# Kernel tuning notes

Measured on AMD Instinct MI355X. Metric: run time of the kernel, lower is better.

Reference implementation:

```python
import jax, jax.numpy as jnp
import numpy as np
import math

B, S, E, H, FF = 2, 2048, 1024, 16, 4096
HD = E // H
EPS = 1e-6


def layer_norm(x, gamma, beta):
    mu = jnp.mean(x, axis=-1, keepdims=True)
    var = jnp.mean(jnp.square(x - mu), axis=-1, keepdims=True)
    return (x - mu) * jax.lax.rsqrt(var + EPS) * gamma + beta


def setup_inputs() -> dict:
    key = jax.random.key(0)
    ks = jax.random.split(key, 8)
    x_embeds = jax.random.normal(ks[0], (B, S, E), dtype=jnp.float32)
    # causal mask: True means masked (j > i), broadcastable over batch/heads
    mask = jnp.triu(jnp.ones((S, S), dtype=bool), k=1)[None, None]
    sc = 1.0 / math.sqrt(E)
    w_kqv = jax.random.normal(ks[1], (3 * E, E), dtype=jnp.float32) * sc
    w_o = jax.random.normal(ks[2], (E, E), dtype=jnp.float32) * sc
    w_up = jax.random.normal(ks[3], (FF, E), dtype=jnp.float32) * sc
    b_up = jnp.zeros((FF,), dtype=jnp.float32)
    w_down = jax.random.normal(ks[4], (E, FF), dtype=jnp.float32) / math.sqrt(FF)
    b_down = jnp.zeros((E,), dtype=jnp.float32)
    g1 = jnp.ones((E,), dtype=jnp.float32)
    b1 = jnp.zeros((E,), dtype=jnp.float32)
    g2 = jnp.ones((E,), dtype=jnp.float32)
    b2 = jnp.zeros((E,), dtype=jnp.float32)
    return {"x_embeds": x_embeds, "mask": mask, "w_kqv": w_kqv, "w_o": w_o,
            "w_up": w_up, "b_up": b_up, "w_down": w_down, "b_down": b_down,
            "g1": g1, "b1": b1, "g2": g2, "b2": b2}


def reference(x_embeds, mask, w_kqv, w_o, w_up, b_up, w_down, b_down, g1, b1, g2, b2):
    b, s = x_embeds.shape[0], x_embeds.shape[1]
    # --- attention ---
    kqv = x_embeds @ w_kqv.T                      # [B,S,3E]
    kqv = kqv.reshape(b, s, 3, H, HD).transpose(0, 3, 2, 1, 4)  # [B,H,3,S,HD]
    xk, xq, xv = kqv[:, :, 0], kqv[:, :, 1], kqv[:, :, 2]
    attn = jnp.einsum('bhqd,bhkd->bhqk', xq, xk) / math.sqrt(HD)
    attn = jnp.where(mask, -jnp.inf, attn)
    attn = jax.nn.softmax(attn, axis=-1)
    out = jnp.einsum('bhqk,bhkd->bhqd', attn, xv)  # [B,H,S,HD]
    out = out.transpose(0, 2, 1, 3).reshape(b, s, E)
    out = out @ w_o.T
    x = layer_norm(out + x_embeds, g1, b1)
    # --- ffnn ---
    h = jax.nn.relu(x @ w_up.T + b_up)
    h = h @ w_down.T + b_down
    return layer_norm(h + x, g2, b2)
```

## Files before the change

kernel.cpp:

```cpp
#include <hip/hip_runtime.h>
#include <stdint.h>

#define B_ 2
#define S_ 2048
#define E_ 1024
#define H_ 16
#define HD_ 64
#define FF_ 4096
#define M_ 4096
#define LOG2E_ 1.44269504f

typedef short bf16x8 __attribute__((ext_vector_type(8)));
typedef float f32x4  __attribute__((ext_vector_type(4)));
typedef short shortx4 __attribute__((ext_vector_type(4)));

#define MFMA16(a,b,c) __builtin_amdgcn_mfma_f32_16x16x32_bf16(a,b,c,0,0,0)

__device__ __forceinline__ short f2bf(float f) {
  uint32_t u = __builtin_bit_cast(uint32_t, f);
  u += 0x7fffu + ((u >> 16) & 1u);
  return (short)(u >> 16);
}
__device__ __forceinline__ float bf2f(short b) {
  uint32_t u = ((uint32_t)(uint16_t)b) << 16;
  return __builtin_bit_cast(float, u);
}
__device__ __forceinline__ float exp2_hw(float x) {
  float r;
  asm("v_exp_f32 %0, %1" : "=v"(r) : "v"(x));
  return r;
}

template<int CTRL>
__device__ __forceinline__ float dpp_ror(float x) {
  return __builtin_bit_cast(float,
    __builtin_amdgcn_update_dpp(0, __builtin_bit_cast(int, x), CTRL, 0xF, 0xF, true));
}
__device__ __forceinline__ float dpp_max16(float v) {
  v = fmaxf(v, dpp_ror<0x128>(v));
  v = fmaxf(v, dpp_ror<0x124>(v));
  v = fmaxf(v, dpp_ror<0x122>(v));
  v = fmaxf(v, dpp_ror<0x121>(v));
  return v;
}
__device__ __forceinline__ float dpp_sum16(float v) {
  v += dpp_ror<0x128>(v);
  v += dpp_ror<0x124>(v);
  v += dpp_ror<0x122>(v);
  v += dpp_ror<0x121>(v);
  return v;
}

#define GLDS16(g, l) __builtin_amdgcn_global_load_lds( \
    (const __attribute__((address_space(1))) unsigned int*)(g), \
    (__attribute__((address_space(3))) unsigned int*)(l), 16, 0, 0)

__global__ void cast_all(const float* __restrict__ x, const float* __restrict__ wkqv,
                         const float* __restrict__ wo, const float* __restrict__ wup,
                         const float* __restrict__ wdown,
                         short* __restrict__ xb, short* __restrict__ wkqvb,
                         short* __restrict__ wob, short* __restrict__ wupb,
                         short* __restrict__ wdownb) {
  const int stride = gridDim.x * blockDim.x;
  for (int i = blockIdx.x * blockDim.x + threadIdx.x; i < 4194304; i += stride) {
    const int e = i << 2;
    const float* src; short* dst; int off;
    if (e < 4194304)       { src = x;     dst = xb;     off = e; }
    else if (e < 7340032)  { src = wkqv;  dst = wkqvb;  off = e - 4194304; }
    else if (e < 8388608)  { src = wo;    dst = wob;    off = e - 7340032; }
    else if (e < 12582912) { src = wup;   dst = wupb;   off = e - 8388608; }
    else                   { src = wdown; dst = wdownb; off = e - 12582912; }
    float4 v = *(const float4*)(src + off);
    shortx4 o;
    o.x = f2bf(v.x); o.y = f2bf(v.y); o.z = f2bf(v.z); o.w = f2bf(v.w);
    *(shortx4*)(dst + off) = o;
  }
}

template<int EPI>
__global__ __launch_bounds__(512, 2) void gemm256_bt(
    const short* __restrict__ A, const short* __restrict__ Bw,
    short* __restrict__ C, const float* __restrict__ bias,
    int M, int N, int K)
{
  __shared__ short Al[2][16384];
  __shared__ short Bl[2][16384];
  const int tid = threadIdx.x;
  const int w = tid >> 6, lane = tid & 63;
  const int lr = lane & 15, lg = lane >> 4;
  const int ntiles = N >> 8;
  const int nwg = gridDim.x;
  const int bid = blockIdx.x;
  const int swz = (bid & 7) * (nwg >> 3) + (bid >> 3);
  const int tn = swz % ntiles, tm = swz / ntiles;
  const int m0 = tm << 8, n0 = tn << 8;
  const int wrm = (w >> 2) << 7;
  const int wcn = (w & 3) << 6;

  const int srow = lane >> 3;
  const int scol = ((lane & 7) ^ srow) << 3;
  const short* Ag[4]; const short* Bg[4];
  #pragma unroll
  for (int i = 0; i < 4; ++i) {
    const int c = w + i * 8;
    Ag[i] = A  + (size_t)(m0 + c * 8 + srow) * K + scol;
    Bg[i] = Bw + (size_t)(n0 + c * 8 + srow) * K + scol;
  }

  f32x4 acc[8][4] = {};
  const int T = K >> 6;

  #pragma unroll
  for (int i = 0; i < 4; ++i) {
    GLDS16(Ag[i], &Al[0][(w + i * 8) * 512]);
    GLDS16(Bg[i], &Bl[0][(w + i * 8) * 512]);
  }

  for (int t = 0; t < T; ++t) {
    const int buf = t & 1;
    const bool more = (t + 1 < T);
    const int k1 = (t + 1) << 6;

    bf16x8 af[8], bf01[4], bf23[4];
    const int ph0 = lg ^ (lr & 7);
    const int ph1 = (4 + lg) ^ (lr & 7);

    if (more) {
      #pragma unroll
      for (int i = 0; i < 4; ++i) {
        GLDS16(Ag[i] + k1, &Al[buf ^ 1][(w + i * 8) * 512]);
        GLDS16(Bg[i] + k1, &Bl[buf ^ 1][(w + i * 8) * 512]);
      }
      asm volatile("s_waitcnt vmcnt(8)" ::: "memory");
    } else {
      asm volatile("s_waitcnt vmcnt(0)" ::: "memory");
    }
    __builtin_amdgcn_sched_barrier(0);
    __builtin_amdgcn_s_barrier();

    #pragma unroll
    for (int i = 0; i < 4; ++i) {
      const int R = wrm + i * 16 + lr;
      af[i * 2]     = *(const bf16x8*)&Al[buf][R * 64 + ph0 * 8];
      af[i * 2 + 1] = *(const bf16x8*)&Al[buf][R * 64 + ph1 * 8];
    }
    #pragma unroll
    for (int j = 0; j < 2; ++j) {
      const int R = wcn + j * 16 + lr;
      bf01[j * 2]     = *(const bf16x8*)&Bl[buf][R * 64 + ph0 * 8];
      bf01[j * 2 + 1] = *(const bf16x8*)&Bl[buf][R * 64 + ph1 * 8];
    }
    __builtin_amdgcn_s_setprio(1);
    #pragma unroll
    for (int i = 0; i < 4; ++i)
      #pragma unroll
      for (int j = 0; j < 2; ++j) {
        acc[i][j] = MFMA16(af[i * 2],     bf01[j * 2],     acc[i][j]);
        acc[i][j] = MFMA16(af[i * 2 + 1], bf01[j * 2 + 1], acc[i][j]);
      }
    __builtin_amdgcn_s_setprio(0);
    __builtin_amdgcn_s_barrier();

    #pragma unroll
    for (int j = 0; j < 2; ++j) {
      const int R = wcn + (j + 2) * 16 + lr;
      bf23[j * 2]     = *(const bf16x8*)&Bl[buf][R * 64 + ph0 * 8];
      bf23[j * 2 + 1] = *(const bf16x8*)&Bl[buf][R * 64 + ph1 * 8];
    }
    __builtin_amdgcn_s_setprio(1);
    #pragma unroll
    for (int i = 0; i < 4; ++i)
      #pragma unroll
      for (int j = 0; j < 2; ++j) {
        acc[i][j + 2] = MFMA16(af[i * 2],     bf23[j * 2],     acc[i][j + 2]);
        acc[i][j + 2] = MFMA16(af[i * 2 + 1], bf23[j * 2 + 1], acc[i][j + 2]);
      }
    __builtin_amdgcn_s_setprio(0);
    __builtin_amdgcn_s_barrier();

    #pragma unroll
    for (int i = 0; i < 4; ++i) {
      const int R = wrm + (i + 4) * 16 + lr;
      af[i * 2]     = *(const bf16x8*)&Al[buf][R * 64 + ph0 * 8];
      af[i * 2 + 1] = *(const bf16x8*)&Al[buf][R * 64 + ph1 * 8];
    }
    __builtin_amdgcn_s_setprio(1);
    #pragma unroll
    for (int i = 0; i < 4; ++i)
      #pragma unroll
      for (int j = 0; j < 2; ++j) {
        acc[i + 4][j + 2] = MFMA16(af[i * 2],     bf23[j * 2],     acc[i + 4][j + 2]);
        acc[i + 4][j + 2] = MFMA16(af[i * 2 + 1], bf23[j * 2 + 1], acc[i + 4][j + 2]);
      }
    __builtin_amdgcn_s_setprio(0);
    __builtin_amdgcn_s_barrier();

    __builtin_amdgcn_s_setprio(1);
    #pragma unroll
    for (int i = 0; i < 4; ++i)
      #pragma unroll
      for (int j = 0; j < 2; ++j) {
        acc[i + 4][j] = MFMA16(af[i * 2],     bf01[j * 2],     acc[i + 4][j]);
        acc[i + 4][j] = MFMA16(af[i * 2 + 1], bf01[j * 2 + 1], acc[i + 4][j]);
      }
    __builtin_amdgcn_s_setprio(0);
    __builtin_amdgcn_s_barrier();
  }

  #pragma unroll
  for (int j = 0; j < 4; ++j) {
    const int col = n0 + wcn + j * 16 + lr;
    float bv = 0.f;
    if constexpr (EPI == 1) bv = bias[col];
    #pragma unroll
    for (int i = 0; i < 8; ++i) {
      #pragma unroll
      for (int r = 0; r < 4; ++r) {
        const int row = m0 + wrm + i * 16 + lg * 4 + r;
        float v = acc[i][j][r] + bv;
        if constexpr (EPI == 1) v = fmaxf(v, 0.f);
        C[(size_t)row * N + col] = f2bf(v);
      }
    }
  }
}

template<int SK, int EPI, typename OutT>
__global__ __launch_bounds__(256) void gemm_bt(
    const short* __restrict__ A, const short* __restrict__ Bw,
    OutT* __restrict__ C0, OutT* __restrict__ C1, const float* __restrict__ bias,
    int M, int N, int K)
{
  __shared__ short Al[2][128 * 32];
  __shared__ short Bl[2][128 * 32];
  const int tid  = threadIdx.x;
  const int w    = tid >> 6, lane = tid & 63;
  const int ntiles = N >> 7;
  const int nwg = gridDim.x;
  const int bid = blockIdx.x;
  const int swz = (bid & 7) * (nwg >> 3) + (bid >> 3);
  const int tn = swz % ntiles, tm = swz / ntiles;
  const int m0 = tm << 7, n0 = tn << 7;
  const int wr = (w >> 1) << 6, wc = (w & 1) << 6;
  const int lr = lane & 15, lk = (lane >> 4) << 3;
  const int ra = lane >> 2, colA = (lane & 3) << 3;

  const int kper = K / SK;
  const int kbeg = (SK > 1) ? (int)blockIdx.y * kper : 0;
  const int T = kper >> 5;
  OutT* __restrict__ C = (SK > 1 && blockIdx.y) ? C1 : C0;

  const short* Ag0 = A  + (size_t)(m0 + w * 16 + ra) * K + colA;
  const short* Ag1 = A  + (size_t)(m0 + (w + 4) * 16 + ra) * K + colA;
  const short* Bg0 = Bw + (size_t)(n0 + w * 16 + ra) * K + colA;
  const short* Bg1 = Bw + (size_t)(n0 + (w + 4) * 16 + ra) * K + colA;

  f32x4 acc[4][4] = {};

  {
    const int k0 = kbeg;
    GLDS16(Ag0 + k0, &Al[0][w * 512]);
    GLDS16(Ag1 + k0, &Al[0][(w + 4) * 512]);
    GLDS16(Bg0 + k0, &Bl[0][w * 512]);
    GLDS16(Bg1 + k0, &Bl[0][(w + 4) * 512]);
  }

  for (int it = 0; it < T; ++it) {
    const int buf = it & 1;
    if (it + 1 < T) {
      const int k1 = kbeg + ((it + 1) << 5);
      GLDS16(Ag0 + k1, &Al[buf ^ 1][w * 512]);
      GLDS16(Ag1 + k1, &Al[buf ^ 1][(w + 4) * 512]);
      GLDS16(Bg0 + k1, &Bl[buf ^ 1][w * 512]);
      GLDS16(Bg1 + k1, &Bl[buf ^ 1][(w + 4) * 512]);
      asm volatile("s_waitcnt vmcnt(4)" ::: "memory");
    } else {
      asm volatile("s_waitcnt vmcnt(0)" ::: "memory");
    }
    __builtin_amdgcn_sched_barrier(0);
    __builtin_amdgcn_s_barrier();

    bf16x8 af[4], bfr[4];
    #pragma unroll
    for (int i = 0; i < 4; ++i)
      af[i] = *(const bf16x8*)&Al[buf][(wr + i * 16 + lr) * 32 + lk];
    #pragma unroll
    for (int j = 0; j < 4; ++j)
      bfr[j] = *(const bf16x8*)&Bl[buf][(wc + j * 16 + lr) * 32 + lk];
    #pragma unroll
    for (int i = 0; i < 4; ++i)
      #pragma unroll
      for (int j = 0; j < 4; ++j)
        acc[i][j] = MFMA16(af[i], bfr[j], acc[i][j]);

    __builtin_amdgcn_s_barrier();
  }

  const int lg = lane >> 4;
  #pragma unroll
  for (int j = 0; j < 4; ++j) {
    const int col = n0 + wc + j * 16 + lr;
    float bv = 0.f;
    if constexpr (SK == 1 && EPI != 0) bv = bias[col];
    #pragma unroll
    for (int i = 0; i < 4; ++i) {
      #pragma unroll
      for (int r = 0; r < 4; ++r) {
        const int row = m0 + wr + i * 16 + lg * 4 + r;
        float v = acc[i][j][r] + bv;
        if constexpr (SK == 1 && EPI == 1) v = fmaxf(v, 0.f);
        if constexpr (sizeof(OutT) == 2) C[(size_t)row * N + col] = f2bf(v);
        else                             C[(size_t)row * N + col] = v;
      }
    }
  }
}

__global__ __launch_bounds__(512) void attn_kernel(
    const short* __restrict__ kqv, short* __restrict__ out)
{
  __shared__ short Kt[2][64][72];
  __shared__ short Vt[2][64][72];
  __shared__ short Pl[8][16][72];

  const int tid = threadIdx.x, w = tid >> 6, lane = tid & 63;
  const int wt = w & 3;
  const int p = blockIdx.x;
  const int bh = blockIdx.y;
  const int b = bh >> 4, h = bh & 15;
  const int q0 = ((w < 4) ? (31 - p) : p) << 6;
  const int nkb = 32 - p;
  const int lr = lane & 15, lg = lane >> 4;

  const size_t rowq = (size_t)(b * S_ + q0 + wt * 16 + lr) * 3072 + 1024 + h * 64;
  bf16x8 qf[2];
  qf[0] = *(const bf16x8*)&kqv[rowq + lg * 8];
  qf[1] = *(const bf16x8*)&kqv[rowq + 32 + lg * 8];
  #pragma unroll
  for (int ks = 0; ks < 2; ++ks)
    #pragma unroll
    for (int e = 0; e < 8; ++e)
      qf[ks][e] = f2bf(bf2f(qf[ks][e]) * 0.125f);

  f32x4 acc[4] = {};
  float m_run[4], l_run[4];
  #pragma unroll
  for (int r = 0; r < 4; ++r) { m_run[r] = -1e30f; l_run[r] = 0.f; }

  const int skk = tid >> 3;
  const int sc  = (tid & 7) << 3;
  const int vws = (tid & 7) << 3;
  const int vkc = skk ^ vws;
  const short* gstage = kqv + (size_t)b * S_ * 3072 + h * 64 + sc;

  {
    bf16x8 kreg = *(const bf16x8*)&gstage[(size_t)skk * 3072];
    bf16x8 vreg = *(const bf16x8*)&gstage[(size_t)skk * 3072 + 2048];
    *(bf16x8*)&Kt[0][skk][sc] = kreg;
    #pragma unroll
    for (int e = 0; e < 8; ++e) Vt[0][sc + e][vkc] = vreg[e];
  }
  __syncthreads();

  for (int kbi = 0; kbi < nkb; ++kbi) {
    const int buf = kbi & 1;
    const int kb = kbi << 6;

    bf16x8 kreg, vreg;
    const bool more = (kbi + 1 < nkb);
    if (more) {
      const size_t gb = (size_t)(((kbi + 1) << 6) + skk) * 3072;
      kreg = *(const bf16x8*)&gstage[gb];
      vreg = *(const bf16x8*)&gstage[gb + 2048];
    }

    if (kb <= q0 + wt * 16 + 15) {
      f32x4 sacc[4] = {};
      __builtin_amdgcn_s_setprio(1);
      #pragma unroll
      for (int jt = 0; jt < 4; ++jt) {
        #pragma unroll
        for (int ks = 0; ks < 2; ++ks) {
          bf16x8 kf = *(const bf16x8*)&Kt[buf][jt * 16 + lr][ks * 32 + lg * 8];
          sacc[jt] = MFMA16(qf[ks], kf, sacc[jt]);
        }
      }
      __builtin_amdgcn_s_setprio(0);
      const bool full = (kb + 63 <= q0 + wt * 16);
      float rmax[4];
      if (full) {
        #pragma unroll
        for (int r = 0; r < 4; ++r)
          rmax[r] = fmaxf(fmaxf(sacc[0][r], sacc[1][r]), fmaxf(sacc[2][r], sacc[3][r]));
      } else {
        #pragma unroll
        for (int r = 0; r < 4; ++r) rmax[r] = -1e30f;
        #pragma unroll
        for (int jt = 0; jt < 4; ++jt) {
          const int kpos = kb + jt * 16 + lr;
          #pragma unroll
          for (int r = 0; r < 4; ++r) {
            const int qrow = q0 + wt * 16 + lg * 4 + r;
            float v = (kpos <= qrow) ? sacc[jt][r] : -1e30f;
            sacc[jt][r] = v;
            rmax[r] = fmaxf(rmax[r], v);
          }
        }
      }
      #pragma unroll
      for (int r = 0; r < 4; ++r) rmax[r] = dpp_max16(rmax[r]);
      int need = 0;
      #pragma unroll
      for (int r = 0; r < 4; ++r) need |= (rmax[r] > m_run[r] + 8.f) ? 1 : 0;
      if (__any(need)) {
        #pragma unroll
        for (int r = 0; r < 4; ++r) {
          const float mn = fmaxf(m_run[r], rmax[r]);
          const float al = exp2_hw((m_run[r] - mn) * LOG2E_);
          m_run[r] = mn;
          l_run[r] *= al;
          #pragma unroll
          for (int dt = 0; dt < 4; ++dt) acc[dt][r] *= al;
        }
      }
      float m2[4], rsum[4];
      #pragma unroll
      for (int r = 0; r < 4; ++r) { m2[r] = m_run[r] * LOG2E_; rsum[r] = 0.f; }
      #pragma unroll
      for (int jt = 0; jt < 4; ++jt)
        #pragma unroll
        for (int r = 0; r < 4; ++r) {
          const float pv = exp2_hw(__builtin_fmaf(sacc[jt][r], LOG2E_, -m2[r]));
          sacc[jt][r] = pv;
          rsum[r] += pv;
        }
      #pragma unroll
      for (int r = 0; r < 4; ++r) { rsum[r] = dpp_sum16(rsum[r]); l_run[r] += rsum[r]; }
      #pragma unroll
      for (int jt = 0; jt < 4; ++jt) {
        uint32_t w01, w23;
        asm("v_cvt_pk_bf16_f32 %0, %1, %2" : "=v"(w01) : "v"(sacc[jt][0]), "v"(sacc[jt][1]));
        asm("v_cvt_pk_bf16_f32 %0, %1, %2" : "=v"(w23) : "v"(sacc[jt][2]), "v"(sacc[jt][3]));
        Pl[w][lg * 4 + 0][jt * 16 + lr] = (short)(w01 & 0xffffu);
        Pl[w][lg * 4 + 1][jt * 16 + lr] = (short)(w01 >> 16);
        Pl[w][lg * 4 + 2][jt * 16 + lr] = (short)(w23 & 0xffffu);
        Pl[w][lg * 4 + 3][jt * 16 + lr] = (short)(w23 >> 16);
      }
      bf16x8 pa[2];
      pa[0] = *(const bf16x8*)&Pl[w][lr][lg * 8];
      pa[1] = *(const bf16x8*)&Pl[w][lr][32 + lg * 8];
      __builtin_amdgcn_s_setprio(1);
      #pragma unroll
      for (int dt = 0; dt < 4; ++dt) {
        const int vswz = (2 * dt + (lr >> 3)) << 3;
        #pragma unroll
        for (int ks = 0; ks < 2; ++ks) {
          bf16x8 vb = *(const bf16x8*)&Vt[buf][dt * 16 + lr][(ks * 32 + lg * 8) ^ vswz];
          acc[dt] = MFMA16(pa[ks], vb, acc[dt]);
        }
      }
      __builtin_amdgcn_s_setprio(0);
    }

    if (more) {
      *(bf16x8*)&Kt[buf ^ 1][skk][sc] = kreg;
      #pragma unroll
      for (int e = 0; e < 8; ++e) Vt[buf ^ 1][sc + e][vkc] = vreg[e];
    }
    __syncthreads();
  }

  #pragma unroll
  for (int dt = 0; dt < 4; ++dt) {
    #pragma unroll
    for (int r = 0; r < 4; ++r) {
      const int d = h * 64 + dt * 16 + lr;
      const int q_row = q0 + wt * 16 + lg * 4 + r;
      out[(size_t)(b * S_ + q_row) * E_ + d] = f2bf(acc[dt][r] / l_run[r]);
    }
  }
}

template<int FINAL>
__global__ __launch_bounds__(256) void ln_kernel(
    const float* __restrict__ y0, const float* __restrict__ y1,
    const float* __restrict__ bias, const void* __restrict__ res,
    const float* __restrict__ gam, const float* __restrict__ bet,
    void* __restrict__ outp)
{
  const int row = blockIdx.x, tid = threadIdx.x, lane = tid & 63, w = tid >> 6;
  float4 a = ((const float4*)(y0 + (size_t)row * E_))[tid];
  float4 c = ((const float4*)(y1 + (size_t)row * E_))[tid];
  float r[4] = {a.x + c.x, a.y + c.y, a.z + c.z, a.w + c.w};
  if constexpr (FINAL) {
    float4 bi = ((const float4*)bias)[tid];
    shortx4 rb = ((const shortx4*)((const short*)res + (size_t)row * E_))[tid];
    r[0] += bi.x + bf2f(rb.x); r[1] += bi.y + bf2f(rb.y);
    r[2] += bi.z + bf2f(rb.z); r[3] += bi.w + bf2f(rb.w);
  } else {
    float4 rv = ((const float4*)((const float*)res + (size_t)row * E_))[tid];
    r[0] += rv.x; r[1] += rv.y; r[2] += rv.z; r[3] += rv.w;
  }
  float s  = r[0] + r[1] + r[2] + r[3];
  float ss = r[0]*r[0] + r[1]*r[1] + r[2]*r[2] + r[3]*r[3];
  #pragma unroll
  for (int m = 32; m >= 1; m >>= 1) { s += __shfl_xor(s, m); ss += __shfl_xor(ss, m); }
  __shared__ float red[8];
  if (lane == 0) { red[w] = s; red[4 + w] = ss; }
  __syncthreads();
  s  = red[0] + red[1] + red[2] + red[3];
  ss = red[4] + red[5] + red[6] + red[7];
  const float mu  = s * (1.f / E_);
  const float var = ss * (1.f / E_) - mu * mu;
  const float rs  = rsqrtf(var + 1e-6f);
  float4 gv = ((const float4*)gam)[tid];
  float4 bv = ((const float4*)bet)[tid];
  float o0 = (r[0] - mu) * rs * gv.x + bv.x;
  float o1 = (r[1] - mu) * rs * gv.y + bv.y;
  float o2 = (r[2] - mu) * rs * gv.z + bv.z;
  float o3 = (r[3] - mu) * rs * gv.w + bv.w;
  if constexpr (FINAL) {
    float4 o; o.x = o0; o.y = o1; o.z = o2; o.w = o3;
    ((float4*)((float*)outp + (size_t)row * E_))[tid] = o;
  } else {
    shortx4 o; o.x = f2bf(o0); o.y = f2bf(o1); o.z = f2bf(o2); o.w = f2bf(o3);
    ((shortx4*)((short*)outp + (size_t)row * E_))[tid] = o;
  }
}

extern "C" void kernel_launch(void* const* d_in, const int* in_sizes, int n_in,
                              void* d_out, int out_size, void* d_ws, size_t ws_size,
                              hipStream_t stream) {
  const float* x      = (const float*)d_in[0];
  const float* w_kqv  = (const float*)d_in[2];
  const float* w_o    = (const float*)d_in[3];
  const float* w_up   = (const float*)d_in[4];
  const float* b_up   = (const float*)d_in[5];
  const float* w_down = (const float*)d_in[6];
  const float* b_down = (const float*)d_in[7];
  const float* g1     = (const float*)d_in[8];
  const float* b1     = (const float*)d_in[9];
  const float* g2     = (const float*)d_in[10];
  const float* b2     = (const float*)d_in[11];
  float* out = (float*)d_out;

  char* ws = (char*)d_ws;
  short* xb     = (short*)(ws);
  short* wkqvb  = (short*)(ws + ((size_t)8  << 20));
  short* wob    = (short*)(ws + ((size_t)14 << 20));
  short* wupb   = (short*)(ws + ((size_t)16 << 20));
  short* wdownb = (short*)(ws + ((size_t)24 << 20));
  short* kqv    = (short*)(ws + ((size_t)32 << 20));
  float* proj0  = (float*)(ws + ((size_t)32 << 20));
  float* proj1  = (float*)(ws + ((size_t)48 << 20));
  short* hbuf   = (short*)(ws + ((size_t)32 << 20));
  short* attno  = (short*)(ws + ((size_t)64 << 20));
  short* xln    = (short*)(ws + ((size_t)72 << 20));
  float* down0  = (float*)(ws);
  float* down1  = (float*)(ws + ((size_t)80 << 20));

  cast_all<<<2048, 256, 0, stream>>>(x, w_kqv, w_o, w_up, w_down,
                                     xb, wkqvb, wob, wupb, wdownb);

  gemm_bt<1, 0, short><<<24 * 32, 256, 0, stream>>>(xb, wkqvb, kqv, nullptr, nullptr, M_, 3 * E_, E_);
  attn_kernel<<<dim3(16, B_ * H_), 512, 0, stream>>>(kqv, attno);
  gemm_bt<2, 0, float><<<dim3(256, 2), 256, 0, stream>>>(attno, wob, proj0, proj1, nullptr, M_, E_, E_);
  ln_kernel<0><<<M_, 256, 0, stream>>>(proj0, proj1, nullptr, x, g1, b1, xln);
  gemm256_bt<1><<<256, 512, 0, stream>>>(xln, wupb, hbuf, b_up, M_, FF_, E_);
  gemm_bt<2, 0, float><<<dim3(256, 2), 256, 0, stream>>>(hbuf, wdownb, down0, down1, nullptr, M_, E_, FF_);
  ln_kernel<1><<<M_, 256, 0, stream>>>(down0, down1, b_down, xln, g2, b2, out);
}
```

Measured before the change: 234.7 us.

## Generalize 256-row GEMM to BN/split-K and use it for out-proj and down-proj

Templates the large 256xBN tiled GEMM on tile width, split-K factor and output type, then uses a 256x128 split-K=2 variant for the attention output projection and the FFN down projection in place of the smaller 128x128 kernel. Larger tiles with 8 waves aim to raise data reuse per LDS load and MFMA density. The trade-off is fewer workgroups (256 total), which may leave some CUs underused, and higher register and LDS pressure per block.

```diff
diff --git a/kernel.cpp b/kernel.cpp
--- a/kernel.cpp
+++ b/kernel.cpp
@@ -77,61 +77,69 @@
   }
 }
 
-template<int EPI>
+template<int BN, int SK, int EPI, typename OutT>
 __global__ __launch_bounds__(512, 2) void gemm256_bt(
     const short* __restrict__ A, const short* __restrict__ Bw,
-    short* __restrict__ C, const float* __restrict__ bias,
+    OutT* __restrict__ C0, OutT* __restrict__ C1, const float* __restrict__ bias,
     int M, int N, int K)
 {
-  __shared__ short Al[2][16384];
-  __shared__ short Bl[2][16384];
+  constexpr int WCN  = BN / 4;
+  constexpr int NJ   = WCN / 16;
+  constexpr int NJH  = NJ / 2;
+  constexpr int ISSB = BN / 64;
+
+  __shared__ short Al[2][256 * 64];
+  __shared__ short Bl[2][BN * 64];
   const int tid = threadIdx.x;
   const int w = tid >> 6, lane = tid & 63;
   const int lr = lane & 15, lg = lane >> 4;
-  const int ntiles = N >> 8;
+  const int ntiles = N / BN;
   const int nwg = gridDim.x;
   const int bid = blockIdx.x;
   const int swz = (bid & 7) * (nwg >> 3) + (bid >> 3);
   const int tn = swz % ntiles, tm = swz / ntiles;
-  const int m0 = tm << 8, n0 = tn << 8;
+  const int m0 = tm << 8, n0 = tn * BN;
   const int wrm = (w >> 2) << 7;
-  const int wcn = (w & 3) << 6;
+  const int wcn = (w & 3) * WCN;
+
+  const int kper = K / SK;
+  const int kbeg = (SK > 1) ? (int)blockIdx.y * kper : 0;
+  const int T = kper >> 6;
+  OutT* __restrict__ C = (SK > 1 && blockIdx.y) ? C1 : C0;
 
   const int srow = lane >> 3;
   const int scol = ((lane & 7) ^ srow) << 3;
-  const short* Ag[4]; const short* Bg[4];
-  #pragma unroll
-  for (int i = 0; i < 4; ++i) {
-    const int c = w + i * 8;
-    Ag[i] = A  + (size_t)(m0 + c * 8 + srow) * K + scol;
-    Bg[i] = Bw + (size_t)(n0 + c * 8 + srow) * K + scol;
-  }
-
-  f32x4 acc[8][4] = {};
-  const int T = K >> 6;
-
-  #pragma unroll
-  for (int i = 0; i < 4; ++i) {
-    GLDS16(Ag[i], &Al[0][(w + i * 8) * 512]);
-    GLDS16(Bg[i], &Bl[0][(w + i * 8) * 512]);
-  }
+  const short* Ag[4]; const short* Bg[ISSB];
+  #pragma unroll
+  for (int i = 0; i < 4; ++i)
+    Ag[i] = A + (size_t)(m0 + (w + i * 8) * 8 + srow) * K + kbeg + scol;
+  #pragma unroll
+  for (int i = 0; i < ISSB; ++i)
+    Bg[i] = Bw + (size_t)(n0 + (w + i * 8) * 8 + srow) * K + kbeg + scol;
+
+  f32x4 acc[8][NJ] = {};
+
+  #pragma unroll
+  for (int i = 0; i < 4; ++i) GLDS16(Ag[i], &Al[0][(w + i * 8) * 512]);
+  #pragma unroll
+  for (int i = 0; i < ISSB; ++i) GLDS16(Bg[i], &Bl[0][(w + i * 8) * 512]);
 
   for (int t = 0; t < T; ++t) {
     const int buf = t & 1;
     const bool more = (t + 1 < T);
     const int k1 = (t + 1) << 6;
 
-    bf16x8 af[8], bf01[4], bf23[4];
+    bf16x8 af[8], bfLo[NJH * 2], bfHi[NJH * 2];
     const int ph0 = lg ^ (lr & 7);
     const int ph1 = (4 + lg) ^ (lr & 7);
 
     if (more) {
       #pragma unroll
-      for (int i = 0; i < 4; ++i) {
-        GLDS16(Ag[i] + k1, &Al[buf ^ 1][(w + i * 8) * 512]);
-        GLDS16(Bg[i] + k1, &Bl[buf ^ 1][(w + i * 8) * 512]);
-      }
-      asm volatile("s_waitcnt vmcnt(8)" ::: "memory");
+      for (int i = 0; i < 4; ++i) GLDS16(Ag[i] + k1, &Al[buf ^ 1][(w + i * 8) * 512]);
+      #pragma unroll
+      for (int i = 0; i < ISSB; ++i) GLDS16(Bg[i] + k1, &Bl[buf ^ 1][(w + i * 8) * 512]);
+      if constexpr (ISSB == 4) asm volatile("s_waitcnt vmcnt(8)" ::: "memory");
+      else                     asm volatile("s_waitcnt vmcnt(6)" ::: "memory");
     } else {
       asm volatile("s_waitcnt vmcnt(0)" ::: "memory");
     }
@@ -145,35 +153,35 @@
       af[i * 2 + 1] = *(const bf16x8*)&Al[buf][R * 64 + ph1 * 8];
     }
     #pragma unroll
-    for (int j = 0; j < 2; ++j) {
+    for (int j = 0; j < NJH; ++j) {
       const int R = wcn + j * 16 + lr;
-      bf01[j * 2]     = *(const bf16x8*)&Bl[buf][R * 64 + ph0 * 8];
-      bf01[j * 2 + 1] = *(const bf16x8*)&Bl[buf][R * 64 + ph1 * 8];
+      bfLo[j * 2]     = *(const bf16x8*)&Bl[buf][R * 64 + ph0 * 8];
+      bfLo[j * 2 + 1] = *(const bf16x8*)&Bl[buf][R * 64 + ph1 * 8];
     }
     __builtin_amdgcn_s_setprio(1);
     #pragma unroll
     for (int i = 0; i < 4; ++i)
       #pragma unroll
-      for (int j = 0; j < 2; ++j) {
-        acc[i][j] = MFMA16(af[i * 2],     bf01[j * 2],     acc[i][j]);
-        acc[i][j] = MFMA16(af[i * 2 + 1], bf01[j * 2 + 1], acc[i][j]);
+      for (int j = 0; j < NJH; ++j) {
+        acc[i][j] = MFMA16(af[i * 2],     bfLo[j * 2],     acc[i][j]);
+        acc[i][j] = MFMA16(af[i * 2 + 1], bfLo[j * 2 + 1], acc[i][j]);
       }
     __builtin_amdgcn_s_setprio(0);
     __builtin_amdgcn_s_barrier();
 
     #pragma unroll
-    for (int j = 0; j < 2; ++j) {
-      const int R = wcn + (j + 2) * 16 + lr;
-      bf23[j * 2]     = *(const bf16x8*)&Bl[buf][R * 64 + ph0 * 8];
-      bf23[j * 2 + 1] = *(const bf16x8*)&Bl[buf][R * 64 + ph1 * 8];
+    for (int j = 0; j < NJH; ++j) {
+      const int R = wcn + (j + NJH) * 16 + lr;
+      bfHi[j * 2]     = *(const bf16x8*)&Bl[buf][R * 64 + ph0 * 8];
+      bfHi[j * 2 + 1] = *(const bf16x8*)&Bl[buf][R * 64 + ph1 * 8];
     }
     __builtin_amdgcn_s_setprio(1);
     #pragma unroll
     for (int i = 0; i < 4; ++i)
       #pragma unroll
-      for (int j = 0; j < 2; ++j) {
-        acc[i][j + 2] = MFMA16(af[i * 2],     bf23[j * 2],     acc[i][j + 2]);
-        acc[i][j + 2] = MFMA16(af[i * 2 + 1], bf23[j * 2 + 1], acc[i][j + 2]);
+      for (int j = 0; j < NJH; ++j) {
+        acc[i][j + NJH] = MFMA16(af[i * 2],     bfHi[j * 2],     acc[i][j + NJH]);
+        acc[i][j + NJH] = MFMA16(af[i * 2 + 1], bfHi[j * 2 + 1], acc[i][j + NJH]);
       }
     __builtin_amdgcn_s_setprio(0);
     __builtin_amdgcn_s_barrier();
@@ -188,9 +196,9 @@
     #pragma unroll
     for (int i = 0; i < 4; ++i)
       #pragma unroll
-      for (int j = 0; j < 2; ++j) {
-        acc[i + 4][j + 2] = MFMA16(af[i * 2],     bf23[j * 2],     acc[i + 4][j + 2]);
-        acc[i + 4][j + 2] = MFMA16(af[i * 2 + 1], bf23[j * 2 + 1], acc[i + 4][j + 2]);
+      for (int j = 0; j < NJH; ++j) {
+        acc[i + 4][j + NJH] = MFMA16(af[i * 2],     bfHi[j * 2],     acc[i + 4][j + NJH]);
+        acc[i + 4][j + NJH] = MFMA16(af[i * 2 + 1], bfHi[j * 2 + 1], acc[i + 4][j + NJH]);
       }
     __builtin_amdgcn_s_setprio(0);
     __builtin_amdgcn_s_barrier();
@@ -199,16 +207,16 @@
     #pragma unroll
     for (int i = 0; i < 4; ++i)
       #pragma unroll
-      for (int j = 0; j < 2; ++j) {
-        acc[i + 4][j] = MFMA16(af[i * 2],     bf01[j * 2],     acc[i + 4][j]);
-        acc[i + 4][j] = MFMA16(af[i * 2 + 1], bf01[j * 2 + 1], acc[i + 4][j]);
+      for (int j = 0; j < NJH; ++j) {
+        acc[i + 4][j] = MFMA16(af[i * 2],     bfLo[j * 2],     acc[i + 4][j]);
+        acc[i + 4][j] = MFMA16(af[i * 2 + 1], bfLo[j * 2 + 1], acc[i + 4][j]);
       }
     __builtin_amdgcn_s_setprio(0);
     __builtin_amdgcn_s_barrier();
   }
 
   #pragma unroll
-  for (int j = 0; j < 4; ++j) {
+  for (int j = 0; j < NJ; ++j) {
     const int col = n0 + wcn + j * 16 + lr;
     float bv = 0.f;
     if constexpr (EPI == 1) bv = bias[col];
@@ -219,7 +227,8 @@
         const int row = m0 + wrm + i * 16 + lg * 4 + r;
         float v = acc[i][j][r] + bv;
         if constexpr (EPI == 1) v = fmaxf(v, 0.f);
-        C[(size_t)row * N + col] = f2bf(v);
+        if constexpr (sizeof(OutT) == 2) C[(size_t)row * N + col] = f2bf(v);
+        else                             C[(size_t)row * N + col] = v;
       }
     }
   }
@@ -564,9 +573,9 @@
 
   gemm_bt<1, 0, short><<<24 * 32, 256, 0, stream>>>(xb, wkqvb, kqv, nullptr, nullptr, M_, 3 * E_, E_);
   attn_kernel<<<dim3(16, B_ * H_), 512, 0, stream>>>(kqv, attno);
-  gemm_bt<2, 0, float><<<dim3(256, 2), 256, 0, stream>>>(attno, wob, proj0, proj1, nullptr, M_, E_, E_);
+  gemm256_bt<128, 2, 0, float><<<dim3(128, 2), 512, 0, stream>>>(attno, wob, proj0, proj1, nullptr, M_, E_, E_);
   ln_kernel<0><<<M_, 256, 0, stream>>>(proj0, proj1, nullptr, x, g1, b1, xln);
-  gemm256_bt<1><<<256, 512, 0, stream>>>(xln, wupb, hbuf, b_up, M_, FF_, E_);
-  gemm_bt<2, 0, float><<<dim3(256, 2), 256, 0, stream>>>(hbuf, wdownb, down0, down1, nullptr, M_, E_, FF_);
+  gemm256_bt<256, 1, 1, short><<<256, 512, 0, stream>>>(xln, wupb, hbuf, (short*)nullptr, b_up, M_, FF_, E_);
+  gemm256_bt<128, 2, 0, float><<<dim3(128, 2), 512, 0, stream>>>(hbuf, wdownb, down0, down1, nullptr, M_, E_, FF_);
   ln_kernel<1><<<M_, 256, 0, stream>>>(down0, down1, b_down, xln, g2, b2, out);
 }
```

Measured after the change: 238.5 us. No clear change (+1.6%).
